# Kernel optimization log

Measured on AMD Instinct MI355X. Metric: run time of the kernel, lower is better.

Reference implementation:

```python
import jax, jax.numpy as jnp
import numpy as np

B, NE, H = 4096, 1024, 256

def setup_inputs() -> dict:
    key = jax.random.key(0)
    k1, k2, k3, k4 = jax.random.split(key, 4)
    x = jax.random.uniform(k1, (B, 2, NE), dtype=jnp.float32)
    W = jax.random.normal(k2, (H, NE), dtype=jnp.float32)
    cov = jax.random.normal(k3, (H, H), dtype=jnp.float32)
    loadings = jax.random.normal(k4, (H, H), dtype=jnp.float32)
    return {"x": x, "W": W, "cov": cov, "loadings": loadings}

def reference(x, W, cov, loadings):
    # values_proj applied to the two slices of x (Linear, no bias)
    values = x[:, 0, :] @ W.T            # [B, H]
    mask = x[:, 1, :] @ W.T              # [B, H]
    one_minus_mask = (1.0 - x[:, 1, :]) @ W.T  # [B, H]
    h = mask.shape[-1]
    # diag_embed(mask) @ cov @ diag_embed(one_minus_mask) == row/col scaling of cov
    wac = jnp.eye(h, dtype=x.dtype) + mask[:, :, None] * cov[None, :, :] * one_minus_mask[:, None, :]  # [B, H, H]
    wac = wac / jnp.sum(wac, axis=-1, keepdims=True)
    wac = jax.nn.softmax(wac, axis=-1)
    L = loadings[None, :, :] * wac       # [B, H, H]
    # values.unsqueeze(1) @ L.transpose(-2,-1) -> out_k = sum_h values_h * L[k, h]
    out = jnp.einsum('bh,bkh->bk', values, L)  # [B, H]
    return out
```

## Files before the change

### kernel.cpp

```cpp
#include <hip/hip_runtime.h>

#define L2E 1.4426950408889634f

__global__ __launch_bounds__(256) void wsum_kernel(const float* __restrict__ W,
                                                   float* __restrict__ wsum) {
    int wave = threadIdx.x >> 6, lane = threadIdx.x & 63;
    int h = blockIdx.x * 4 + wave;
    const float* row = W + (size_t)h * 1024;
    float s = 0.f;
#pragma unroll
    for (int i = 0; i < 16; ++i) s += row[lane + 64 * i];
#pragma unroll
    for (int off = 32; off; off >>= 1) s += __shfl_xor(s, off, 64);
    if (lane == 0) wsum[h] = s;
}

__global__ __launch_bounds__(256) void prep_kernel(const float* __restrict__ cov,
                                                   const float* __restrict__ ld,
                                                   float* __restrict__ covT0,
                                                   float2* __restrict__ clT) {
    __shared__ float tc[32][33];
    __shared__ float tl[32][33];
    const int bx = blockIdx.x * 32, by = blockIdx.y * 32;
    const int x = threadIdx.x & 31;
    const int y = threadIdx.x >> 5;
#pragma unroll
    for (int i = 0; i < 32; i += 8) {
        int r = by + y + i, c = bx + x;
        float cv = cov[(size_t)r * 256 + c];
        float lv = ld[(size_t)r * 256 + c];
        if (r == c) { cv = 0.f; lv = 0.f; }
        tc[y + i][x] = cv; tl[y + i][x] = lv;
    }
    __syncthreads();
#pragma unroll
    for (int i = 0; i < 32; i += 8) {
        int r = bx + y + i, c = by + x;
        float cv = tc[x][y + i], lv = tl[x][y + i];
        covT0[(size_t)r * 256 + c] = cv;
        clT[(size_t)r * 256 + c] = make_float2(cv, lv);
    }
}

#define BM 64
#define BN 64
#define BK 16
#define LDT 68

__global__ __launch_bounds__(256) void gemm_kernel(const float* __restrict__ X,
                                                   const float* __restrict__ W,
                                                   float* __restrict__ C) {
    __shared__ float As[BK][LDT];
    __shared__ float Bs[BK][LDT];
    const int tid = threadIdx.x;
    const int row = tid >> 2;
    const int c4  = (tid & 3) << 2;
    const int gm0 = blockIdx.x * BM;
    const int gn0 = blockIdx.y * BN;
    const int tx = tid & 15, ty = tid >> 4;
    float acc[4][4] = {};
    const float* Xp = X + (size_t)(gm0 + row) * 1024 + c4;
    const float* Wp = W + (size_t)(gn0 + row) * 1024 + c4;

    float4 a = *(const float4*)(Xp);
    float4 b = *(const float4*)(Wp);
    for (int kt = 0; kt < 1024; kt += BK) {
        __syncthreads();
        As[c4 + 0][row] = a.x; As[c4 + 1][row] = a.y;
        As[c4 + 2][row] = a.z; As[c4 + 3][row] = a.w;
        Bs[c4 + 0][row] = b.x; Bs[c4 + 1][row] = b.y;
        Bs[c4 + 2][row] = b.z; Bs[c4 + 3][row] = b.w;
        __syncthreads();
        if (kt + BK < 1024) {
            a = *(const float4*)(Xp + kt + BK);
            b = *(const float4*)(Wp + kt + BK);
        }
#pragma unroll
        for (int kk = 0; kk < BK; ++kk) {
            float4 av = *(const float4*)&As[kk][ty << 2];
            float4 bv = *(const float4*)&Bs[kk][tx << 2];
            float am[4] = {av.x, av.y, av.z, av.w};
            float bn[4] = {bv.x, bv.y, bv.z, bv.w};
#pragma unroll
            for (int i = 0; i < 4; ++i)
#pragma unroll
                for (int j = 0; j < 4; ++j)
                    acc[i][j] = __builtin_fmaf(am[i], bn[j], acc[i][j]);
        }
    }
#pragma unroll
    for (int i = 0; i < 4; ++i) {
        float4 o = {acc[i][0], acc[i][1], acc[i][2], acc[i][3]};
        *(float4*)(C + (size_t)(gm0 + (ty << 2) + i) * 256 + gn0 + (tx << 2)) = o;
    }
}

#define NB 4

__global__ __launch_bounds__(256) void head_kernel(const float* __restrict__ C,
                                                   const float* __restrict__ wsum,
                                                   const float* __restrict__ covT0,
                                                   const float2* __restrict__ clT,
                                                   const float* __restrict__ cov,
                                                   const float* __restrict__ ld,
                                                   float* __restrict__ out) {
    __shared__ float  omm[NB][256];
    __shared__ float2 pv[NB][256];
    const int k = threadIdx.x;
    const int b0 = blockIdx.x * NB;

    const float ws = wsum[k];
    const float cdiag = cov[(size_t)k * 257];
    const float ldiag = ld[(size_t)k * 257];

    float mk[NB], vak[NB], omk[NB], sp[NB], pmax[NB], pmin[NB];
#pragma unroll
    for (int b = 0; b < NB; ++b) {
        float va = C[(size_t)(2 * (b0 + b)) * 256 + k];
        float ms = C[(size_t)(2 * (b0 + b) + 1) * 256 + k];
        float o  = ws - ms;
        mk[b] = ms; vak[b] = va; omk[b] = o;
        omm[b][k] = o;
        pv[b][k] = make_float2(o, va);
        sp[b] = 0.f; pmax[b] = 0.f; pmin[b] = 0.f;
    }
    __syncthreads();

#pragma unroll 8
    for (int j = 0; j < 256; ++j) {
        float cv = covT0[j * 256 + k];
#pragma unroll
        for (int b = 0; b < NB; ++b) {
            float p = cv * omm[b][j];
            sp[b]   += p;
            pmax[b]  = fmaxf(pmax[b], p);
            pmin[b]  = fminf(pmin[b], p);
        }
    }

    float c1[NB], c0[NB], ek[NB], se[NB], dp[NB];
#pragma unroll
    for (int b = 0; b < NB; ++b) {
        float m   = mk[b];
        float pkk = cdiag * omk[b];
        float rkk = __builtin_fmaf(m, pkk, 1.0f);
        float sum = __builtin_fmaf(m, sp[b] + pkk, 1.0f);
        float iv  = __builtin_amdgcn_rcpf(sum);
        float rmax = (m >= 0.f) ? m * pmax[b] : m * pmin[b];
        float rmin = (m >= 0.f) ? m * pmin[b] : m * pmax[b];
        rmax = fmaxf(rmax, rkk);
        rmin = fminf(rmin, rkk);
        float mx = (iv >= 0.f) ? iv * rmax : iv * rmin;
        c1[b] = m * iv * L2E;
        c0[b] = -mx * L2E;
        ek[b] = __builtin_amdgcn_exp2f(__builtin_fmaf(rkk * iv, L2E, c0[b]));
        se[b] = 0.f; dp[b] = 0.f;
    }

#pragma unroll 8
    for (int j = 0; j < 256; ++j) {
        float2 cl = clT[j * 256 + k];
#pragma unroll
        for (int b = 0; b < NB; ++b) {
            float2 ov = pv[b][j];
            float p = cl.x * ov.x;
            float e = __builtin_amdgcn_exp2f(__builtin_fmaf(p, c1[b], c0[b]));
            se[b] += e;
            dp[b]  = __builtin_fmaf(e, cl.y * ov.y, dp[b]);
        }
    }

#pragma unroll
    for (int b = 0; b < NB; ++b) {
        float espur = __builtin_amdgcn_exp2f(c0[b]);
        float sef = se[b] + (ek[b] - espur);
        float dpf = __builtin_fmaf(ek[b], ldiag * vak[b], dp[b]);
        out[(size_t)(b0 + b) * 256 + k] = dpf * __builtin_amdgcn_rcpf(sef);
    }
}

extern "C" void kernel_launch(void* const* d_in, const int* in_sizes, int n_in,
                              void* d_out, int out_size, void* d_ws, size_t ws_size,
                              hipStream_t stream) {
    const float* x    = (const float*)d_in[0];
    const float* W    = (const float*)d_in[1];
    const float* cov  = (const float*)d_in[2];
    const float* ldng = (const float*)d_in[3];
    float* out = (float*)d_out;

    float*  C     = (float*)d_ws;
    float*  wsum  = C + (size_t)8192 * 256;
    float*  covT0 = wsum + 256;
    float2* clT   = (float2*)(covT0 + 65536);

    wsum_kernel<<<64, 256, 0, stream>>>(W, wsum);
    prep_kernel<<<dim3(8, 8), 256, 0, stream>>>(cov, ldng, covT0, clT);
    gemm_kernel<<<dim3(128, 4), 256, 0, stream>>>(x, W, C);
    head_kernel<<<1024, 256, 0, stream>>>(C, wsum, covT0, clT, cov, ldng, out);
}
```

Baseline: 149.9 us.

## Double-buffer GEMM shared-memory tiles and widen K step to 32

The projection GEMM now uses two shared-memory buffers per operand and a K tile of 32 instead of 16. Each thread loads 8 floats per row per step, so the next tile is stored while the current one is computed. This cuts the barriers to one per iteration and halves the iteration count. The cost is doubled LDS (about 34 KB per block) and more registers, which may reduce occupancy.

New measurement: 155.9 us. +4.0%, slower.

```diff
diff --git a/kernel.cpp b/kernel.cpp
--- a/kernel.cpp
+++ b/kernel.cpp
@@ -42,43 +42,64 @@
     }
 }
 
-#define BM 64
-#define BN 64
-#define BK 16
+#define GBK 32
 #define LDT 68
 
 __global__ __launch_bounds__(256) void gemm_kernel(const float* __restrict__ X,
                                                    const float* __restrict__ W,
                                                    float* __restrict__ C) {
-    __shared__ float As[BK][LDT];
-    __shared__ float Bs[BK][LDT];
+    __shared__ float As[2][GBK][LDT];
+    __shared__ float Bs[2][GBK][LDT];
     const int tid = threadIdx.x;
     const int row = tid >> 2;
-    const int c4  = (tid & 3) << 2;
-    const int gm0 = blockIdx.x * BM;
-    const int gn0 = blockIdx.y * BN;
+    const int k0  = (tid & 3) << 3;
+    const int gm0 = blockIdx.x * 64;
+    const int gn0 = blockIdx.y * 64;
     const int tx = tid & 15, ty = tid >> 4;
     float acc[4][4] = {};
-    const float* Xp = X + (size_t)(gm0 + row) * 1024 + c4;
-    const float* Wp = W + (size_t)(gn0 + row) * 1024 + c4;
-
-    float4 a = *(const float4*)(Xp);
-    float4 b = *(const float4*)(Wp);
-    for (int kt = 0; kt < 1024; kt += BK) {
-        __syncthreads();
-        As[c4 + 0][row] = a.x; As[c4 + 1][row] = a.y;
-        As[c4 + 2][row] = a.z; As[c4 + 3][row] = a.w;
-        Bs[c4 + 0][row] = b.x; Bs[c4 + 1][row] = b.y;
-        Bs[c4 + 2][row] = b.z; Bs[c4 + 3][row] = b.w;
-        __syncthreads();
-        if (kt + BK < 1024) {
-            a = *(const float4*)(Xp + kt + BK);
-            b = *(const float4*)(Wp + kt + BK);
-        }
-#pragma unroll
-        for (int kk = 0; kk < BK; ++kk) {
-            float4 av = *(const float4*)&As[kk][ty << 2];
-            float4 bv = *(const float4*)&Bs[kk][tx << 2];
+    const float* Xp = X + (size_t)(gm0 + row) * 1024 + k0;
+    const float* Wp = W + (size_t)(gn0 + row) * 1024 + k0;
+
+    float4 xa = *(const float4*)(Xp);
+    float4 xb = *(const float4*)(Xp + 4);
+    float4 wa = *(const float4*)(Wp);
+    float4 wb = *(const float4*)(Wp + 4);
+
+#define WRBUF(B)                                                        \
+    {                                                                   \
+        As[B][k0 + 0][row] = xa.x; As[B][k0 + 1][row] = xa.y;           \
+        As[B][k0 + 2][row] = xa.z; As[B][k0 + 3][row] = xa.w;           \
+        As[B][k0 + 4][row] = xb.x; As[B][k0 + 5][row] = xb.y;           \
+        As[B][k0 + 6][row] = xb.z; As[B][k0 + 7][row] = xb.w;           \
+        Bs[B][k0 + 0][row] = wa.x; Bs[B][k0 + 1][row] = wa.y;           \
+        Bs[B][k0 + 2][row] = wa.z; Bs[B][k0 + 3][row] = wa.w;           \
+        Bs[B][k0 + 4][row] = wb.x; Bs[B][k0 + 5][row] = wb.y;           \
+        Bs[B][k0 + 6][row] = wb.z; Bs[B][k0 + 7][row] = wb.w;           \
+    }
+
+    WRBUF(0);
+    xa = *(const float4*)(Xp + GBK);
+    xb = *(const float4*)(Xp + GBK + 4);
+    wa = *(const float4*)(Wp + GBK);
+    wb = *(const float4*)(Wp + GBK + 4);
+    __syncthreads();
+
+    int cur = 0;
+    for (int it = 0; it < 32; ++it) {
+        if (it < 31) {
+            if (cur == 0) WRBUF(1) else WRBUF(0);
+        }
+        if (it < 30) {
+            int off = (it + 2) * GBK;
+            xa = *(const float4*)(Xp + off);
+            xb = *(const float4*)(Xp + off + 4);
+            wa = *(const float4*)(Wp + off);
+            wb = *(const float4*)(Wp + off + 4);
+        }
+#pragma unroll
+        for (int kk = 0; kk < GBK; ++kk) {
+            float4 av = *(const float4*)&As[cur][kk][ty << 2];
+            float4 bv = *(const float4*)&Bs[cur][kk][tx << 2];
             float am[4] = {av.x, av.y, av.z, av.w};
             float bn[4] = {bv.x, bv.y, bv.z, bv.w};
 #pragma unroll
@@ -87,12 +108,15 @@
                 for (int j = 0; j < 4; ++j)
                     acc[i][j] = __builtin_fmaf(am[i], bn[j], acc[i][j]);
         }
+        __syncthreads();
+        cur ^= 1;
     }
 #pragma unroll
     for (int i = 0; i < 4; ++i) {
         float4 o = {acc[i][0], acc[i][1], acc[i][2], acc[i][3]};
         *(float4*)(C + (size_t)(gm0 + (ty << 2) + i) * 256 + gn0 + (tx << 2)) = o;
     }
+#undef WRBUF
 }
 
 #define NB 4
```
